# Optimization experiments

Hardware: AMD Instinct MI355X
Metric: run time of the kernel (lower is better)

The kernel has to match this reference:

```python
import jax, jax.numpy as jnp
import numpy as np

B, C, W, H = 4, 64, 64, 64
CH = 64  # ch == input_nc so residual is valid

def setup_inputs() -> dict:
    key = jax.random.key(0)
    ks = jax.random.split(key, 5)
    return {
        "x": jax.random.normal(ks[0], (B, C, W, H), jnp.float32),
        "y": jax.random.normal(ks[1], (B, C, W, H), jnp.float32),
        "Wf": jax.random.normal(ks[2], (CH // 2, C), jnp.float32) * 0.05,
        "bf": jnp.zeros((CH // 2,), jnp.float32),
        "Wg": jax.random.normal(ks[3], (CH // 2, C), jnp.float32) * 0.05,
        "bg": jnp.zeros((CH // 2,), jnp.float32),
        "Wh": jax.random.normal(ks[4], (CH, C), jnp.float32) * 0.05,
        "bh": jnp.zeros((CH,), jnp.float32),
        "gamma": jnp.full((1,), 0.5, jnp.float32),
    }

def reference(x, y, Wf, bf, Wg, bg, Wh, bh, gamma):
    b, c, w, h = x.shape
    n = w * h
    xf = x.reshape(b, c, n)   # [b, C, N]
    yf = y.reshape(b, c, n)
    # 1x1 convs == per-pixel linear maps over channels
    f = jnp.einsum('oc,bcn->bon', Wf, xf) + bf[None, :, None]   # [b, CH/2, N]
    g = jnp.einsum('oc,bcn->bon', Wg, yf) + bg[None, :, None]   # [b, CH/2, N]
    hv = jnp.einsum('oc,bcn->bon', Wh, yf) + bh[None, :, None]  # [b, CH,   N]
    # s = g^T @ f : [b, N, N]
    s = jnp.einsum('bcm,bcn->bmn', g, f)
    beta = jax.nn.softmax(s, axis=-1)
    # o = beta @ h^T : [b, N, CH]
    o = jnp.einsum('bmn,bcn->bmc', beta, hv)
    o = o.transpose(0, 2, 1).reshape(b, -1, w, h)  # [b, CH, w, h]
    return gamma[0] * o + x
```

## Files before the change

kernel.cpp:

```cpp
#include <hip/hip_runtime.h>
#include <hip/hip_bf16.h>

#define BB  4
#define CC  64
#define NN  4096
#define CF  32
#define CHN 64

#define LOG2E 1.4426950408889634f

typedef __attribute__((ext_vector_type(8)))  __bf16 bf16x8;
typedef __attribute__((ext_vector_type(4)))  __bf16 bf16x4;
typedef __attribute__((ext_vector_type(4)))  float  floatx4;
typedef __attribute__((ext_vector_type(16))) float  floatx16;
typedef __attribute__((ext_vector_type(2)))  unsigned int uintx2;
typedef __attribute__((ext_vector_type(4)))  unsigned int uintx4;

__device__ __forceinline__ float scrub(float v) {
    return fminf(fmaxf(v, -1e30f), 1e30f);
}

__device__ __forceinline__ unsigned cvt_pk_bf16(float lo, float hi) {
    unsigned r;
    asm("v_cvt_pk_bf16_f32 %0, %1, %2" : "=v"(r) : "v"(lo), "v"(hi));
    return r;
}
__device__ __forceinline__ float exp2_f32(float x) {
    float r;
    asm("v_exp_f32 %0, %1" : "=v"(r) : "v"(x));
    return r;
}


__global__ __launch_bounds__(256) void prep_kernel(
    const float* __restrict__ x, const float* __restrict__ y,
    const float* __restrict__ Wf, const float* __restrict__ bfp,
    const float* __restrict__ Wg, const float* __restrict__ bgp,
    const float* __restrict__ Wh, const float* __restrict__ bhp,
    __bf16* __restrict__ fT, __bf16* __restrict__ gT, __bf16* __restrict__ hvb)
{
    __shared__ __align__(16) __bf16 wbf[128][72];
    __shared__ float sbias[128];

    const int t  = threadIdx.x;
    const int w  = t >> 6;
    const int l  = t & 63;
    const int lo = l & 15;
    const int q  = l >> 4;

    const int b   = blockIdx.x >> 7;
    const int nb  = blockIdx.x & 127;
    const int nn  = nb * 32 + (w & 1) * 16 + lo;
    const int ctbase = (w < 2) ? 0 : 4;

    for (int i = t; i < 128 * CC; i += 256) {
        int row = i >> 6, c = i & 63;
        float wv;
        if (row < 32)      wv = Wf[(size_t)row * CC + c];
        else if (row < 64) wv = Wg[(size_t)(row - 32) * CC + c];
        else               wv = Wh[(size_t)(row - 64) * CC + c];
        wbf[row][c] = (__bf16)wv;
    }
    if (t < 128) {
        if (t < 32)      sbias[t] = bfp[t];
        else if (t < 64) sbias[t] = bgp[t - 32];
        else             sbias[t] = bhp[t - 64];
    }
    __syncthreads();

    const float* xb = x + (size_t)b * CC * NN;
    const float* yb = y + (size_t)b * CC * NN;
    bf16x8 bx[2], by[2];
    #pragma unroll
    for (int kh = 0; kh < 2; kh++)
        #pragma unroll
        for (int j = 0; j < 8; j++) {
            int c = kh * 32 + q * 8 + j;
            by[kh][j] = (__bf16)yb[(size_t)c * NN + nn];
        }
    if (ctbase == 0) {
        #pragma unroll
        for (int kh = 0; kh < 2; kh++)
            #pragma unroll
            for (int j = 0; j < 8; j++) {
                int c = kh * 32 + q * 8 + j;
                bx[kh][j] = (__bf16)xb[(size_t)c * NN + nn];
            }
    }

    const floatx4 zero4 = {0.f, 0.f, 0.f, 0.f};
    #pragma unroll
    for (int cti = 0; cti < 4; cti++) {
        const int ct = ctbase + cti;
        const bf16x8* src = (ct < 2) ? bx : by;
        floatx4 acc = zero4;
        #pragma unroll
        for (int kh = 0; kh < 2; kh++) {
            const bf16x8 a = *(const bf16x8*)&wbf[ct*16 + lo][kh*32 + q*8];
            acc = __builtin_amdgcn_mfma_f32_16x16x32_bf16(a, src[kh], acc, 0, 0, 0);
        }
        if (ct < 4) {
            const float sc = (ct < 2) ? 1.0f : LOG2E;
            bf16x4 pk;
            #pragma unroll
            for (int r = 0; r < 4; r++)
                pk[r] = (__bf16)((acc[r] + sbias[ct*16 + q*4 + r]) * sc);
            __bf16* dstbase = (ct < 2) ? fT : gT;
            const int c0 = (ct & 1) * 16 + q * 4;
            const int off = (nn >> 5)*1024 + (c0 >> 4)*512 + (nn & 31)*16
                          + ((c0 >> 3) & 1)*8 + (c0 & 7);
            *(bf16x4*)&dstbase[(size_t)b * NN * CF + off] = pk;
        } else {
            #pragma unroll
            for (int r = 0; r < 4; r++) {
                int ch = (ct - 4) * 16 + q*4 + r;
                const int off = (nn >> 6)*4096 + (ch >> 5)*2048
                              + ((nn >> 4) & 3)*512 + (ch & 31)*16
                              + ((nn >> 3) & 1)*8 + (nn & 7);
                hvb[(size_t)b * CHN * NN + off] =
                    (__bf16)(acc[r] + sbias[64 + ch]);
            }
        }
    }
}

__global__ __launch_bounds__(512, 2) void attn_kernel(
    const __bf16* __restrict__ fT, const __bf16* __restrict__ gT,
    const __bf16* __restrict__ hvb,
    const float* __restrict__ x, const float* __restrict__ gamma_p,
    float* __restrict__ out)
{
    __shared__ float osum[8][64][67];
    __shared__ float lsum[512];

    const int t   = threadIdx.x;
    const int w   = t >> 6;
    const int l   = t & 63;
    const int l31 = l & 31;
    const int hi  = l >> 5;

    const int slot = blockIdx.x;
    const int xcd  = slot & 7;
    const int b    = xcd >> 1;
    const int mg   = ((xcd & 1) << 5) | (slot >> 3);
    const int m0   = mg * 64;

    const __bf16* fb = fT  + (size_t)b * NN * CF;
    const __bf16* gb = gT  + (size_t)b * NN * CF;
    const __bf16* hb = hvb + (size_t)b * CHN * NN;

    const int lane16 = (l31 * 2 + hi) * 8;

    bf16x8 bg_[2][2];
    #pragma unroll
    for (int mt = 0; mt < 2; mt++)
        #pragma unroll
        for (int kk = 0; kk < 2; kk++)
            bg_[mt][kk] = *(const bf16x8*)(gb + (size_t)(mg*2 + mt)*1024 + kk*512 + lane16);

    const floatx16 zero16 = {};
    floatx16 oacc[2][2];
    #pragma unroll
    for (int mt = 0; mt < 2; mt++)
        #pragma unroll
        for (int ct = 0; ct < 2; ct++) oacc[mt][ct] = zero16;
    float rsum[2] = {0.f, 0.f};

    for (int i = 0; i < 8; i++) {
        const int nc = 8*i + w;

        bf16x8 af[2][2];
        #pragma unroll
        for (int nt = 0; nt < 2; nt++)
            #pragma unroll
            for (int kk = 0; kk < 2; kk++)
                af[nt][kk] = *(const bf16x8*)(fb + (size_t)(nc*2 + nt)*1024 + kk*512 + lane16);

        bf16x8 bv[2][4];
        #pragma unroll
        for (int ct = 0; ct < 2; ct++)
            #pragma unroll
            for (int ks = 0; ks < 4; ks++)
                bv[ct][ks] = *(const bf16x8*)(hb + (size_t)nc*4096 + ct*2048 + ks*512 + lane16);

        bf16x8 pa[2][4];
        #pragma unroll
        for (int mt = 0; mt < 2; mt++) {
            #pragma unroll
            for (int nt = 0; nt < 2; nt++) {
                floatx16 s = __builtin_amdgcn_mfma_f32_32x32x16_bf16(
                    af[nt][0], bg_[mt][0], zero16, 0, 0, 0);
                s = __builtin_amdgcn_mfma_f32_32x32x16_bf16(
                    af[nt][1], bg_[mt][1], s, 0, 0, 0);

                float p[16];
                #pragma unroll
                for (int r = 0; r < 16; r++) p[r] = exp2_f32(s[r]);

                #pragma unroll
                for (int r = 0; r < 16; r++) rsum[mt] += p[r];

                unsigned W[8];
                #pragma unroll
                for (int g = 0; g < 8; g++) W[g] = cvt_pk_bf16(p[2*g], p[2*g+1]);

                uintx2 s02 = __builtin_amdgcn_permlane32_swap(W[0], W[2], false, false);
                uintx2 s13 = __builtin_amdgcn_permlane32_swap(W[1], W[3], false, false);
                uintx2 s46 = __builtin_amdgcn_permlane32_swap(W[4], W[6], false, false);
                uintx2 s57 = __builtin_amdgcn_permlane32_swap(W[5], W[7], false, false);

                uintx4 w0 = {s02.x, s13.x, s02.y, s13.y};
                uintx4 w1 = {s46.x, s57.x, s46.y, s57.y};
                pa[mt][nt*2 + 0] = __builtin_bit_cast(bf16x8, w0);
                pa[mt][nt*2 + 1] = __builtin_bit_cast(bf16x8, w1);
            }
        }

        #pragma unroll
        for (int mt = 0; mt < 2; mt++)
            #pragma unroll
            for (int ct = 0; ct < 2; ct++)
                #pragma unroll
                for (int ks = 0; ks < 4; ks++)
                    oacc[mt][ct] = __builtin_amdgcn_mfma_f32_32x32x16_bf16(
                        pa[mt][ks], bv[ct][ks], oacc[mt][ct], 0, 0, 0);
    }

    #pragma unroll
    for (int mt = 0; mt < 2; mt++)
        rsum[mt] += __shfl_xor(rsum[mt], 32, 64);

    #pragma unroll
    for (int mt = 0; mt < 2; mt++) {
        #pragma unroll
        for (int ct = 0; ct < 2; ct++)
            #pragma unroll
            for (int r = 0; r < 16; r++)
                osum[w][mt*32 + ((r&3) + 8*(r>>2) + 4*hi)][ct*32 + l31] =
                    oacc[mt][ct][r];
        if (hi == 0)
            lsum[w*64 + mt*32 + l31] = rsum[mt];
    }
    __syncthreads();

    const float gam = gamma_p[0];
    const int m  = t & 63;
    const int cb = t >> 6;
    float lt = 0.f;
    #pragma unroll
    for (int s = 0; s < 8; s++) lt += lsum[s*64 + m];
    const float inv = 1.f / lt;
    #pragma unroll
    for (int it = 0; it < 8; it++) {
        const int ch = it*8 + cb;
        float acc = 0.f;
        #pragma unroll
        for (int s = 0; s < 8; s++) acc += osum[s][m][ch];
        size_t gi = ((size_t)b * CHN + ch) * NN + m0 + m;
        float ov = scrub(acc * inv);
        out[gi] = gam * ov + x[gi];
    }
}

extern "C" void kernel_launch(void* const* d_in, const int* in_sizes, int n_in,
                              void* d_out, int out_size, void* d_ws, size_t ws_size,
                              hipStream_t stream)
{
    const float* x     = (const float*)d_in[0];
    const float* y     = (const float*)d_in[1];
    const float* Wf    = (const float*)d_in[2];
    const float* bf    = (const float*)d_in[3];
    const float* Wg    = (const float*)d_in[4];
    const float* bg    = (const float*)d_in[5];
    const float* Wh    = (const float*)d_in[6];
    const float* bh    = (const float*)d_in[7];
    const float* gamma = (const float*)d_in[8];
    float* out = (float*)d_out;

    __bf16* wsb = (__bf16*)d_ws;
    __bf16* fT  = wsb;
    __bf16* gT  = fT + (size_t)BB * NN * CF;
    __bf16* hvb = gT + (size_t)BB * NN * CF;

    prep_kernel<<<dim3(BB * 128), dim3(256), 0, stream>>>(
        x, y, Wf, bf, Wg, bg, Wh, bh, fT, gT, hvb);
    attn_kernel<<<dim3(BB * 64), dim3(512), 0, stream>>>(
        fT, gT, hvb, x, gamma, out);
}
```

Before: 92.79 us.

## Split attention m-tiles across twice as many waves per block

The attention kernel now launches 1024 threads per block instead of 512. The two 32-row m-tiles that each wave used to process are split across two wave groups, so every wave keeps a single score tile and a single set of output accumulators. This halves per-wave register pressure and doubles the waves per CU available to hide MFMA and exp latency. In exchange, both wave groups load the same f and h fragments, and the tighter launch bounds may push the compiler to spill registers.

```diff
diff --git a/kernel.cpp b/kernel.cpp
--- a/kernel.cpp
+++ b/kernel.cpp
@@ -124,7 +124,7 @@
     }
 }
 
-__global__ __launch_bounds__(512, 2) void attn_kernel(
+__global__ __launch_bounds__(1024, 4) void attn_kernel(
     const __bf16* __restrict__ fT, const __bf16* __restrict__ gT,
     const __bf16* __restrict__ hvb,
     const float* __restrict__ x, const float* __restrict__ gamma_p,
@@ -135,6 +135,8 @@
 
     const int t   = threadIdx.x;
     const int w   = t >> 6;
+    const int pw  = w & 7;
+    const int mh  = w >> 3;
     const int l   = t & 63;
     const int l31 = l & 31;
     const int hi  = l >> 5;
@@ -151,23 +153,19 @@
 
     const int lane16 = (l31 * 2 + hi) * 8;
 
-    bf16x8 bg_[2][2];
-    #pragma unroll
-    for (int mt = 0; mt < 2; mt++)
-        #pragma unroll
-        for (int kk = 0; kk < 2; kk++)
-            bg_[mt][kk] = *(const bf16x8*)(gb + (size_t)(mg*2 + mt)*1024 + kk*512 + lane16);
+    bf16x8 bg_[2];
+    #pragma unroll
+    for (int kk = 0; kk < 2; kk++)
+        bg_[kk] = *(const bf16x8*)(gb + (size_t)(mg*2 + mh)*1024 + kk*512 + lane16);
 
     const floatx16 zero16 = {};
-    floatx16 oacc[2][2];
-    #pragma unroll
-    for (int mt = 0; mt < 2; mt++)
-        #pragma unroll
-        for (int ct = 0; ct < 2; ct++) oacc[mt][ct] = zero16;
-    float rsum[2] = {0.f, 0.f};
+    floatx16 oacc[2];
+    #pragma unroll
+    for (int ct = 0; ct < 2; ct++) oacc[ct] = zero16;
+    float rsum = 0.f;
 
     for (int i = 0; i < 8; i++) {
-        const int nc = 8*i + w;
+        const int nc = 8*i + pw;
 
         bf16x8 af[2][2];
         #pragma unroll
@@ -176,6 +174,36 @@
             for (int kk = 0; kk < 2; kk++)
                 af[nt][kk] = *(const bf16x8*)(fb + (size_t)(nc*2 + nt)*1024 + kk*512 + lane16);
 
+        bf16x8 pa[4];
+        #pragma unroll
+        for (int nt = 0; nt < 2; nt++) {
+            floatx16 s = __builtin_amdgcn_mfma_f32_32x32x16_bf16(
+                af[nt][0], bg_[0], zero16, 0, 0, 0);
+            s = __builtin_amdgcn_mfma_f32_32x32x16_bf16(
+                af[nt][1], bg_[1], s, 0, 0, 0);
+
+            float p[16];
+            #pragma unroll
+            for (int r = 0; r < 16; r++) p[r] = exp2_f32(s[r]);
+
+            #pragma unroll
+            for (int r = 0; r < 16; r++) rsum += p[r];
+
+            unsigned W[8];
+            #pragma unroll
+            for (int g = 0; g < 8; g++) W[g] = cvt_pk_bf16(p[2*g], p[2*g+1]);
+
+            uintx2 s02 = __builtin_amdgcn_permlane32_swap(W[0], W[2], false, false);
+            uintx2 s13 = __builtin_amdgcn_permlane32_swap(W[1], W[3], false, false);
+            uintx2 s46 = __builtin_amdgcn_permlane32_swap(W[4], W[6], false, false);
+            uintx2 s57 = __builtin_amdgcn_permlane32_swap(W[5], W[7], false, false);
+
+            uintx4 w0 = {s02.x, s13.x, s02.y, s13.y};
+            uintx4 w1 = {s46.x, s57.x, s46.y, s57.y};
+            pa[nt*2 + 0] = __builtin_bit_cast(bf16x8, w0);
+            pa[nt*2 + 1] = __builtin_bit_cast(bf16x8, w1);
+        }
+
         bf16x8 bv[2][4];
         #pragma unroll
         for (int ct = 0; ct < 2; ct++)
@@ -183,64 +211,24 @@
             for (int ks = 0; ks < 4; ks++)
                 bv[ct][ks] = *(const bf16x8*)(hb + (size_t)nc*4096 + ct*2048 + ks*512 + lane16);
 
-        bf16x8 pa[2][4];
-        #pragma unroll
-        for (int mt = 0; mt < 2; mt++) {
-            #pragma unroll
-            for (int nt = 0; nt < 2; nt++) {
-                floatx16 s = __builtin_amdgcn_mfma_f32_32x32x16_bf16(
-                    af[nt][0], bg_[mt][0], zero16, 0, 0, 0);
-                s = __builtin_amdgcn_mfma_f32_32x32x16_bf16(
-                    af[nt][1], bg_[mt][1], s, 0, 0, 0);
-
-                float p[16];
-                #pragma unroll
-                for (int r = 0; r < 16; r++) p[r] = exp2_f32(s[r]);
-
-                #pragma unroll
-                for (int r = 0; r < 16; r++) rsum[mt] += p[r];
-
-                unsigned W[8];
-                #pragma unroll
-                for (int g = 0; g < 8; g++) W[g] = cvt_pk_bf16(p[2*g], p[2*g+1]);
-
-                uintx2 s02 = __builtin_amdgcn_permlane32_swap(W[0], W[2], false, false);
-                uintx2 s13 = __builtin_amdgcn_permlane32_swap(W[1], W[3], false, false);
-                uintx2 s46 = __builtin_amdgcn_permlane32_swap(W[4], W[6], false, false);
-                uintx2 s57 = __builtin_amdgcn_permlane32_swap(W[5], W[7], false, false);
-
-                uintx4 w0 = {s02.x, s13.x, s02.y, s13.y};
-                uintx4 w1 = {s46.x, s57.x, s46.y, s57.y};
-                pa[mt][nt*2 + 0] = __builtin_bit_cast(bf16x8, w0);
-                pa[mt][nt*2 + 1] = __builtin_bit_cast(bf16x8, w1);
-            }
-        }
-
-        #pragma unroll
-        for (int mt = 0; mt < 2; mt++)
-            #pragma unroll
-            for (int ct = 0; ct < 2; ct++)
-                #pragma unroll
-                for (int ks = 0; ks < 4; ks++)
-                    oacc[mt][ct] = __builtin_amdgcn_mfma_f32_32x32x16_bf16(
-                        pa[mt][ks], bv[ct][ks], oacc[mt][ct], 0, 0, 0);
-    }
-
-    #pragma unroll
-    for (int mt = 0; mt < 2; mt++)
-        rsum[mt] += __shfl_xor(rsum[mt], 32, 64);
-
-    #pragma unroll
-    for (int mt = 0; mt < 2; mt++) {
         #pragma unroll
         for (int ct = 0; ct < 2; ct++)
             #pragma unroll
-            for (int r = 0; r < 16; r++)
-                osum[w][mt*32 + ((r&3) + 8*(r>>2) + 4*hi)][ct*32 + l31] =
-                    oacc[mt][ct][r];
-        if (hi == 0)
-            lsum[w*64 + mt*32 + l31] = rsum[mt];
-    }
+            for (int ks = 0; ks < 4; ks++)
+                oacc[ct] = __builtin_amdgcn_mfma_f32_32x32x16_bf16(
+                    pa[ks], bv[ct][ks], oacc[ct], 0, 0, 0);
+    }
+
+    rsum += __shfl_xor(rsum, 32, 64);
+
+    #pragma unroll
+    for (int ct = 0; ct < 2; ct++)
+        #pragma unroll
+        for (int r = 0; r < 16; r++)
+            osum[pw][mh*32 + ((r&3) + 8*(r>>2) + 4*hi)][ct*32 + l31] =
+                oacc[ct][r];
+    if (hi == 0)
+        lsum[pw*64 + mh*32 + l31] = rsum;
     __syncthreads();
 
     const float gam = gamma_p[0];
@@ -251,8 +239,8 @@
     for (int s = 0; s < 8; s++) lt += lsum[s*64 + m];
     const float inv = 1.f / lt;
     #pragma unroll
-    for (int it = 0; it < 8; it++) {
-        const int ch = it*8 + cb;
+    for (int it = 0; it < 4; it++) {
+        const int ch = it*16 + cb;
         float acc = 0.f;
         #pragma unroll
         for (int s = 0; s < 8; s++) acc += osum[s][m][ch];
@@ -284,6 +272,6 @@
 
     prep_kernel<<<dim3(BB * 128), dim3(256), 0, stream>>>(
         x, y, Wf, bf, Wg, bg, Wh, bh, fT, gT, hvb);
-    attn_kernel<<<dim3(BB * 64), dim3(512), 0, stream>>>(
+    attn_kernel<<<dim3(BB * 64), dim3(1024), 0, stream>>>(
         fT, gT, hvb, x, gamma, out);
 }
```

New measurement: 96.31 us. +3.8%, slower.

## Split key dimension across block pairs with global partial-sum combine

Applied to the files above, without the earlier changes.

Each block now covers 128 query rows over half of the key range, not 64 rows over all keys. Two blocks on adjacent XCDs split the keys and write partial outputs and row sums to a workspace buffer. An atomic pair counter lets the second finisher combine both halves, normalise and write the output. This doubles reuse of each loaded f and h tile across query tiles, at the cost of extra global traffic, fences, and a serialized combine step in half of the blocks.

```diff
diff --git a/kernel.cpp b/kernel.cpp
--- a/kernel.cpp
+++ b/kernel.cpp
@@ -30,6 +30,8 @@
     asm("v_exp_f32 %0, %1" : "=v"(r) : "v"(x));
     return r;
 }
+
+__device__ unsigned pair_cnt[128];
 
 
 __global__ __launch_bounds__(256) void prep_kernel(
@@ -126,12 +128,13 @@
 
 __global__ __launch_bounds__(512, 2) void attn_kernel(
     const __bf16* __restrict__ fT, const __bf16* __restrict__ gT,
-    const __bf16* __restrict__ hvb,
+    const __bf16* __restrict__ hvb, float* __restrict__ pbuf,
     const float* __restrict__ x, const float* __restrict__ gamma_p,
     float* __restrict__ out)
 {
     __shared__ float osum[8][64][67];
     __shared__ float lsum[512];
+    __shared__ int   sflag;
 
     const int t   = threadIdx.x;
     const int w   = t >> 6;
@@ -142,8 +145,10 @@
     const int slot = blockIdx.x;
     const int xcd  = slot & 7;
     const int b    = xcd >> 1;
-    const int mg   = ((xcd & 1) << 5) | (slot >> 3);
-    const int m0   = mg * 64;
+    const int half = xcd & 1;
+    const int tm   = slot >> 3;
+    const int pair = slot >> 1;
+    const int m0   = tm * 128;
 
     const __bf16* fb = fT  + (size_t)b * NN * CF;
     const __bf16* gb = gT  + (size_t)b * NN * CF;
@@ -151,23 +156,24 @@
 
     const int lane16 = (l31 * 2 + hi) * 8;
 
-    bf16x8 bg_[2][2];
-    #pragma unroll
-    for (int mt = 0; mt < 2; mt++)
+    bf16x8 bg_[4][2];
+    #pragma unroll
+    for (int mt = 0; mt < 4; mt++)
         #pragma unroll
         for (int kk = 0; kk < 2; kk++)
-            bg_[mt][kk] = *(const bf16x8*)(gb + (size_t)(mg*2 + mt)*1024 + kk*512 + lane16);
+            bg_[mt][kk] = *(const bf16x8*)(gb + (size_t)(tm*4 + mt)*1024 + kk*512 + lane16);
 
     const floatx16 zero16 = {};
-    floatx16 oacc[2][2];
-    #pragma unroll
-    for (int mt = 0; mt < 2; mt++)
+    floatx16 oacc[4][2];
+    #pragma unroll
+    for (int mt = 0; mt < 4; mt++)
         #pragma unroll
         for (int ct = 0; ct < 2; ct++) oacc[mt][ct] = zero16;
-    float rsum[2] = {0.f, 0.f};
-
-    for (int i = 0; i < 8; i++) {
-        const int nc = 8*i + w;
+    float rsum[4] = {0.f, 0.f, 0.f, 0.f};
+
+    #pragma unroll
+    for (int i = 0; i < 4; i++) {
+        const int nc = half*32 + 8*i + w;
 
         bf16x8 af[2][2];
         #pragma unroll
@@ -183,9 +189,9 @@
             for (int ks = 0; ks < 4; ks++)
                 bv[ct][ks] = *(const bf16x8*)(hb + (size_t)nc*4096 + ct*2048 + ks*512 + lane16);
 
-        bf16x8 pa[2][4];
-        #pragma unroll
-        for (int mt = 0; mt < 2; mt++) {
+        #pragma unroll
+        for (int mt = 0; mt < 4; mt++) {
+            bf16x8 pa[4];
             #pragma unroll
             for (int nt = 0; nt < 2; nt++) {
                 floatx16 s = __builtin_amdgcn_mfma_f32_32x32x16_bf16(
@@ -211,54 +217,79 @@
 
                 uintx4 w0 = {s02.x, s13.x, s02.y, s13.y};
                 uintx4 w1 = {s46.x, s57.x, s46.y, s57.y};
-                pa[mt][nt*2 + 0] = __builtin_bit_cast(bf16x8, w0);
-                pa[mt][nt*2 + 1] = __builtin_bit_cast(bf16x8, w1);
+                pa[nt*2 + 0] = __builtin_bit_cast(bf16x8, w0);
+                pa[nt*2 + 1] = __builtin_bit_cast(bf16x8, w1);
             }
-        }
-
-        #pragma unroll
-        for (int mt = 0; mt < 2; mt++)
             #pragma unroll
             for (int ct = 0; ct < 2; ct++)
                 #pragma unroll
                 for (int ks = 0; ks < 4; ks++)
                     oacc[mt][ct] = __builtin_amdgcn_mfma_f32_32x32x16_bf16(
-                        pa[mt][ks], bv[ct][ks], oacc[mt][ct], 0, 0, 0);
-    }
-
-    #pragma unroll
-    for (int mt = 0; mt < 2; mt++)
+                        pa[ks], bv[ct][ks], oacc[mt][ct], 0, 0, 0);
+        }
+    }
+
+    #pragma unroll
+    for (int mt = 0; mt < 4; mt++)
         rsum[mt] += __shfl_xor(rsum[mt], 32, 64);
 
-    #pragma unroll
-    for (int mt = 0; mt < 2; mt++) {
-        #pragma unroll
-        for (int ct = 0; ct < 2; ct++)
-            #pragma unroll
-            for (int r = 0; r < 16; r++)
-                osum[w][mt*32 + ((r&3) + 8*(r>>2) + 4*hi)][ct*32 + l31] =
-                    oacc[mt][ct][r];
-        if (hi == 0)
-            lsum[w*64 + mt*32 + l31] = rsum[mt];
+    const size_t PSTR = 128*64 + 128;
+    float* myO = pbuf + ((size_t)pair*2 + half) * PSTR;
+    float* myL = myO + 128*64;
+    float* otO = pbuf + ((size_t)pair*2 + (half^1)) * PSTR;
+    float* otL = otO + 128*64;
+
+    #pragma unroll
+    for (int mp = 0; mp < 2; mp++) {
+        if (mp) __syncthreads();
+        #pragma unroll
+        for (int mtl = 0; mtl < 2; mtl++) {
+            const int mt = mp*2 + mtl;
+            #pragma unroll
+            for (int ct = 0; ct < 2; ct++)
+                #pragma unroll
+                for (int r = 0; r < 16; r++)
+                    osum[w][mtl*32 + ((r&3) + 8*(r>>2) + 4*hi)][ct*32 + l31] =
+                        oacc[mt][ct][r];
+            if (hi == 0)
+                lsum[w*64 + mtl*32 + l31] = rsum[mt];
+        }
+        __syncthreads();
+        #pragma unroll
+        for (int it = 0; it < 8; it++) {
+            const int idx = it*512 + t;
+            const int m  = idx & 63;
+            const int ch = idx >> 6;
+            float a = 0.f;
+            #pragma unroll
+            for (int s = 0; s < 8; s++) a += osum[s][m][ch];
+            myO[ch*128 + mp*64 + m] = a;
+        }
+        if (t < 64) {
+            float a = 0.f;
+            #pragma unroll
+            for (int s = 0; s < 8; s++) a += lsum[s*64 + t];
+            myL[mp*64 + t] = a;
+        }
     }
     __syncthreads();
-
+    __threadfence();
+    if (t == 0) sflag = (int)(atomicAdd(&pair_cnt[pair], 1u) & 1u);
+    __syncthreads();
+    if (sflag == 0) return;
+    __threadfence();
+
+    if (t < 128) lsum[t] = 1.f / (myL[t] + otL[t]);
+    __syncthreads();
     const float gam = gamma_p[0];
-    const int m  = t & 63;
-    const int cb = t >> 6;
-    float lt = 0.f;
-    #pragma unroll
-    for (int s = 0; s < 8; s++) lt += lsum[s*64 + m];
-    const float inv = 1.f / lt;
-    #pragma unroll
-    for (int it = 0; it < 8; it++) {
-        const int ch = it*8 + cb;
-        float acc = 0.f;
-        #pragma unroll
-        for (int s = 0; s < 8; s++) acc += osum[s][m][ch];
+    #pragma unroll
+    for (int it = 0; it < 16; it++) {
+        const int idx = it*512 + t;
+        const int m  = idx & 127;
+        const int ch = idx >> 7;
+        float O = myO[ch*128 + m] + otO[ch*128 + m];
         size_t gi = ((size_t)b * CHN + ch) * NN + m0 + m;
-        float ov = scrub(acc * inv);
-        out[gi] = gam * ov + x[gi];
+        out[gi] = gam * scrub(O * lsum[m]) + x[gi];
     }
 }
 
@@ -281,9 +312,10 @@
     __bf16* fT  = wsb;
     __bf16* gT  = fT + (size_t)BB * NN * CF;
     __bf16* hvb = gT + (size_t)BB * NN * CF;
+    float* pbuf = (float*)(hvb + (size_t)BB * CHN * NN);
 
     prep_kernel<<<dim3(BB * 128), dim3(256), 0, stream>>>(
         x, y, Wf, bf, Wg, bg, Wh, bh, fT, gT, hvb);
     attn_kernel<<<dim3(BB * 64), dim3(512), 0, stream>>>(
-        fT, gT, hvb, x, gamma, out);
-}
+        fT, gT, hvb, pbuf, x, gamma, out);
+}
```

After: 153.7 us. 1.66x slower.

## Split attention key range across two blocks with atomic last-arriver combine

Applied to the files above, without the earlier changes.

Each 64-query tile's key loop is split in half across two blocks, doubling the grid to 512 blocks and raising the occupancy hint to 4 blocks per CU. Each block reduces its waves' partial outputs and row sums in shared memory, writes them to a global scratch buffer, and increments a per-pair atomic counter. The second block to arrive, detected by counter parity, adds both partials, normalizes and writes the residual output. The aim is to fill more of the GPU and hide latency, at the cost of extra global writes, fences and a serialized combine step; the shared osum buffer is halved and reused in two phases.

```diff
diff --git a/kernel.cpp b/kernel.cpp
--- a/kernel.cpp
+++ b/kernel.cpp
@@ -30,6 +30,8 @@
     asm("v_exp_f32 %0, %1" : "=v"(r) : "v"(x));
     return r;
 }
+
+__device__ unsigned pair_cnt[256];
 
 
 __global__ __launch_bounds__(256) void prep_kernel(
@@ -124,14 +126,15 @@
     }
 }
 
-__global__ __launch_bounds__(512, 2) void attn_kernel(
+__global__ __launch_bounds__(512, 4) void attn_kernel(
     const __bf16* __restrict__ fT, const __bf16* __restrict__ gT,
-    const __bf16* __restrict__ hvb,
+    const __bf16* __restrict__ hvb, float* __restrict__ pbuf,
     const float* __restrict__ x, const float* __restrict__ gamma_p,
     float* __restrict__ out)
 {
-    __shared__ float osum[8][64][67];
+    __shared__ float osum[8][32][67];
     __shared__ float lsum[512];
+    __shared__ int   sflag;
 
     const int t   = threadIdx.x;
     const int w   = t >> 6;
@@ -142,8 +145,10 @@
     const int slot = blockIdx.x;
     const int xcd  = slot & 7;
     const int b    = xcd >> 1;
-    const int mg   = ((xcd & 1) << 5) | (slot >> 3);
+    const int half = xcd & 1;
+    const int mg   = slot >> 3;
     const int m0   = mg * 64;
+    const int pair = mg * 4 + b;
 
     const __bf16* fb = fT  + (size_t)b * NN * CF;
     const __bf16* gb = gT  + (size_t)b * NN * CF;
@@ -166,8 +171,9 @@
         for (int ct = 0; ct < 2; ct++) oacc[mt][ct] = zero16;
     float rsum[2] = {0.f, 0.f};
 
-    for (int i = 0; i < 8; i++) {
-        const int nc = 8*i + w;
+    #pragma unroll
+    for (int i = 0; i < 4; i++) {
+        const int nc = half*32 + 8*i + w;
 
         bf16x8 af[2][2];
         #pragma unroll
@@ -230,35 +236,58 @@
     for (int mt = 0; mt < 2; mt++)
         rsum[mt] += __shfl_xor(rsum[mt], 32, 64);
 
+    const size_t PSTR = 64*64 + 64;
+    float* myO = pbuf + ((size_t)pair*2 + half) * PSTR;
+    float* myL = myO + 64*64;
+    const float* otO = pbuf + ((size_t)pair*2 + (half^1)) * PSTR;
+    const float* otL = otO + 64*64;
+
     #pragma unroll
     for (int mt = 0; mt < 2; mt++) {
+        if (mt) __syncthreads();
         #pragma unroll
         for (int ct = 0; ct < 2; ct++)
             #pragma unroll
             for (int r = 0; r < 16; r++)
-                osum[w][mt*32 + ((r&3) + 8*(r>>2) + 4*hi)][ct*32 + l31] =
-                    oacc[mt][ct][r];
+                osum[w][(r&3) + 8*(r>>2) + 4*hi][ct*32 + l31] = oacc[mt][ct][r];
         if (hi == 0)
             lsum[w*64 + mt*32 + l31] = rsum[mt];
+        __syncthreads();
+        #pragma unroll
+        for (int it = 0; it < 4; it++) {
+            const int idx = it*512 + t;
+            const int mr = idx & 31;
+            const int ch = idx >> 5;
+            float a = 0.f;
+            #pragma unroll
+            for (int s = 0; s < 8; s++) a += osum[s][mr][ch];
+            myO[ch*64 + mt*32 + mr] = a;
+        }
+    }
+    if (t < 64) {
+        float a = 0.f;
+        #pragma unroll
+        for (int s = 0; s < 8; s++) a += lsum[s*64 + t];
+        myL[t] = a;
     }
     __syncthreads();
-
+    __threadfence();
+    if (t == 0) sflag = (int)(atomicAdd(&pair_cnt[pair], 1u) & 1u);
+    __syncthreads();
+    if (sflag == 0) return;
+    __threadfence();
+
+    if (t < 64) lsum[t] = 1.f / (myL[t] + otL[t]);
+    __syncthreads();
     const float gam = gamma_p[0];
-    const int m  = t & 63;
-    const int cb = t >> 6;
-    float lt = 0.f;
-    #pragma unroll
-    for (int s = 0; s < 8; s++) lt += lsum[s*64 + m];
-    const float inv = 1.f / lt;
     #pragma unroll
     for (int it = 0; it < 8; it++) {
-        const int ch = it*8 + cb;
-        float acc = 0.f;
-        #pragma unroll
-        for (int s = 0; s < 8; s++) acc += osum[s][m][ch];
+        const int idx = it*512 + t;
+        const int m  = idx & 63;
+        const int ch = idx >> 6;
+        float O = myO[ch*64 + m] + otO[ch*64 + m];
         size_t gi = ((size_t)b * CHN + ch) * NN + m0 + m;
-        float ov = scrub(acc * inv);
-        out[gi] = gam * ov + x[gi];
+        out[gi] = gam * scrub(O * lsum[m]) + x[gi];
     }
 }
 
@@ -281,9 +310,10 @@
     __bf16* fT  = wsb;
     __bf16* gT  = fT + (size_t)BB * NN * CF;
     __bf16* hvb = gT + (size_t)BB * NN * CF;
+    float* pbuf = (float*)(hvb + (size_t)BB * CHN * NN);
 
     prep_kernel<<<dim3(BB * 128), dim3(256), 0, stream>>>(
         x, y, Wf, bf, Wg, bg, Wh, bh, fT, gT, hvb);
-    attn_kernel<<<dim3(BB * 64), dim3(512), 0, stream>>>(
-        fT, gT, hvb, x, gamma, out);
-}
+    attn_kernel<<<dim3(BB * 128), dim3(512), 0, stream>>>(
+        fT, gT, hvb, pbuf, x, gamma, out);
+}
```

Result: slower. 338.5 us (+264.8%).
